# Kernel optimization log

Measured on AMD Instinct MI355X. Metric: run time of the kernel, lower is better.

## Reference

```python
import jax, jax.numpy as jnp
import numpy as np

EPS = 1e-4
LN_EPS = 1e-5
N, E, D_IN, D_HID, D_OUT = 100000, 1600000, 128, 256, 128


def _layer_norm(x, g, b):
    m = jnp.mean(x, axis=-1, keepdims=True)
    v = jnp.mean(jnp.square(x - m), axis=-1, keepdims=True)
    return (x - m) * jax.lax.rsqrt(v + LN_EPS) * g + b


def setup_inputs() -> dict:
    key = jax.random.key(0)
    ks = jax.random.split(key, 10)
    x = jax.random.normal(ks[0], (N, D_IN), dtype=jnp.float32)
    edge_index = jax.random.randint(ks[1], (2, E), 0, N, dtype=jnp.int64)
    degree = jax.random.uniform(ks[2], (N,), dtype=jnp.float32) * 32.0
    s_in = 1.0 / np.sqrt(D_IN)
    s_hid = 1.0 / np.sqrt(D_HID)
    return {
        "x": x,
        "edge_index": edge_index,
        "degree": degree,
        # fc: Linear(in_dim, out_dim, bias=True)
        "W_fc": jax.random.normal(ks[3], (D_OUT, D_IN), dtype=jnp.float32) * s_in,
        "b_fc": jnp.zeros((D_OUT,), dtype=jnp.float32),
        # rate: Linear(in_dim, out_dim, bias=False)
        "W_rate": jax.random.normal(ks[4], (D_OUT, D_IN), dtype=jnp.float32) * s_in,
        # rob_bound: Linear(in,hid)+Softplus -> Linear(hid,out) -> LayerNorm(out)
        "W1": jax.random.normal(ks[5], (D_HID, D_IN), dtype=jnp.float32) * s_in,
        "b1": jnp.zeros((D_HID,), dtype=jnp.float32),
        "W2": jax.random.normal(ks[6], (D_OUT, D_HID), dtype=jnp.float32) * s_hid,
        "b2": jnp.zeros((D_OUT,), dtype=jnp.float32),
        "ln1_g": jnp.ones((D_OUT,), dtype=jnp.float32),
        "ln1_b": jnp.zeros((D_OUT,), dtype=jnp.float32),
        # final self.norm LayerNorm(out)
        "ln2_g": jnp.ones((D_OUT,), dtype=jnp.float32),
        "ln2_b": jnp.zeros((D_OUT,), dtype=jnp.float32),
    }


def reference(x, edge_index, degree, W_fc, b_fc, W_rate, W1, b1, W2, b2,
              ln1_g, ln1_b, ln2_g, ln2_b):
    # rate = Softplus(x @ W_rate^T)   (dropout = identity in eval)
    rate = jax.nn.softplus(jnp.einsum('nd,od->no', x, W_rate))
    # gamma = LayerNorm(Softplus(x @ W1^T + b1) @ W2^T + b2)
    h = jax.nn.softplus(jnp.einsum('nd,hd->nh', x, W1) + b1)
    gamma = _layer_norm(jnp.einsum('nh,oh->no', h, W2) + b2, ln1_g, ln1_b)
    # z = fc(x)
    z = jnp.einsum('nd,od->no', x, W_fc) + b_fc
    row, col = edge_index[0], edge_index[1]
    # edge gather + scatter-sum back onto source nodes (row)
    msg = z[row] + z[col]                                   # [E, D_OUT]
    agg = jax.ops.segment_sum(msg, row, num_segments=N)     # [N, D_OUT]
    out = (rate * agg + gamma) / (1.0 + rate * degree[:, None] + EPS) - z
    out = _layer_norm(out, ln2_g, ln2_b)
    return out  # act = Identity, dropout = identity (eval)
```

## Files before the change

### kernel.cpp

```cpp
#include <hip/hip_runtime.h>
#include <hip/hip_bf16.h>
#include <stdint.h>


typedef __attribute__((ext_vector_type(8))) short  sh8;
typedef __attribute__((ext_vector_type(4))) float  f32x4;

__device__ __forceinline__ float softplus_fast(float v) {
    const float t = __expf(-fabsf(v));
    return fmaxf(v, 0.0f) + __logf(1.0f + t);
}
__device__ __forceinline__ unsigned short f2b(float f) {
    unsigned int u = __float_as_uint(f);
    u += 0x7fffu + ((u >> 16) & 1u);
    return (unsigned short)(u >> 16);
}
__device__ __forceinline__ float b2lo(unsigned int u) {
    return __uint_as_float(u << 16);
}
__device__ __forceinline__ float b2hi(unsigned int u) {
    return __uint_as_float(u & 0xffff0000u);
}

__global__ __launch_bounds__(256)
void convert_pad(const float* __restrict__ x, unsigned short* __restrict__ xb,
                 long long n_valid, long long n_total)
{
    long long i = ((long long)blockIdx.x * blockDim.x + threadIdx.x) * 8;
    const long long stride = (long long)gridDim.x * blockDim.x * 8;
    for (; i < n_total; i += stride) {
        sh8 o;
        if (i + 8 <= n_valid) {
            const float4 f0 = *(const float4*)(x + i);
            const float4 f1 = *(const float4*)(x + i + 4);
            o[0] = (short)f2b(f0.x); o[1] = (short)f2b(f0.y);
            o[2] = (short)f2b(f0.z); o[3] = (short)f2b(f0.w);
            o[4] = (short)f2b(f1.x); o[5] = (short)f2b(f1.y);
            o[6] = (short)f2b(f1.z); o[7] = (short)f2b(f1.w);
        } else {
            o = (sh8)(short)0;
        }
        *(sh8*)(xb + i) = o;
    }
}

__global__ __launch_bounds__(256)
void convert_weights(const float* __restrict__ Wfc, const float* __restrict__ Wrt,
                     const float* __restrict__ W1,  const float* __restrict__ W2,
                     unsigned short* __restrict__ wb)
{
    const int i = blockIdx.x * blockDim.x + threadIdx.x;
    float v;
    if (i < 16384)       v = Wfc[i];
    else if (i < 32768)  v = Wrt[i - 16384];
    else if (i < 65536)  v = W1[i - 32768];
    else                 v = W2[i - 65536];
    wb[i] = f2b(v);
}


__global__ __launch_bounds__(256)
void gemm_fused3(const unsigned short* __restrict__ A, const unsigned short* __restrict__ Wcat,
                 const float* __restrict__ b_fc, const float* __restrict__ b1,
                 unsigned short* __restrict__ zbuf, unsigned short* __restrict__ rbuf,
                 unsigned short* __restrict__ hbuf)
{
    __shared__ unsigned short As[128 * 64];
    __shared__ unsigned short Bs[128 * 64];
    const int tid  = threadIdx.x;
    const int lane = tid & 63;
    const int w    = tid >> 6;
    const int wr   = w >> 1, wc = w & 1;
    const int row0 = blockIdx.x * 128;
    const int by   = blockIdx.y;
    const int col0 = by * 128;
    const int K    = 128;

    f32x4 acc[4][4];
    const f32x4 vzero = {0.f, 0.f, 0.f, 0.f};
    #pragma unroll
    for (int m = 0; m < 4; ++m)
        #pragma unroll
        for (int n = 0; n < 4; ++n) acc[m][n] = vzero;

    for (int kt = 0; kt < K; kt += 64) {
        #pragma unroll
        for (int c = 0; c < 4; ++c) {
            const int idx = c * 256 + tid;
            const int row = idx >> 3;
            const int gs  = (idx & 7) ^ (row & 7);
            __builtin_amdgcn_global_load_lds(
                (const __attribute__((address_space(1))) void*)(A + (size_t)(row0 + row) * K + kt + gs * 8),
                (__attribute__((address_space(3))) void*)(As + idx * 8), 16, 0, 0);
        }
        #pragma unroll
        for (int c = 0; c < 4; ++c) {
            const int idx = c * 256 + tid;
            const int row = idx >> 3;
            const int gs  = (idx & 7) ^ (row & 7);
            __builtin_amdgcn_global_load_lds(
                (const __attribute__((address_space(1))) void*)(Wcat + (size_t)(col0 + row) * K + kt + gs * 8),
                (__attribute__((address_space(3))) void*)(Bs + idx * 8), 16, 0, 0);
        }
        __syncthreads();

        #pragma unroll
        for (int kk = 0; kk < 2; ++kk) {
            const int gg = kk * 4 + (lane >> 4);
            sh8 a[4], b[4];
            #pragma unroll
            for (int m = 0; m < 4; ++m) {
                const int r = wr * 64 + m * 16 + (lane & 15);
                a[m] = *(const sh8*)(As + r * 64 + ((gg ^ (r & 7)) << 3));
            }
            #pragma unroll
            for (int n = 0; n < 4; ++n) {
                const int r = wc * 64 + n * 16 + (lane & 15);
                b[n] = *(const sh8*)(Bs + r * 64 + ((gg ^ (r & 7)) << 3));
            }
            #pragma unroll
            for (int m = 0; m < 4; ++m)
                #pragma unroll
                for (int n = 0; n < 4; ++n)
                    acc[m][n] = __builtin_amdgcn_mfma_f32_16x16x32_bf16(a[m], b[n], acc[m][n], 0, 0, 0);
        }
        __syncthreads();
    }

    unsigned short* dst;
    int ldc, cbase, mode;
    if (by == 0)      { dst = zbuf; ldc = 128; cbase = 0;   mode = 0; }
    else if (by == 1) { dst = rbuf; ldc = 128; cbase = 0;   mode = 1; }
    else              { dst = hbuf; ldc = 256; cbase = col0 - 256; mode = 2; }

    float bs[4];
    #pragma unroll
    for (int n = 0; n < 4; ++n) {
        const int cw = col0 + wc * 64 + n * 16 + (lane & 15);
        bs[n] = (mode == 0) ? b_fc[cw] : (mode == 2 ? b1[cw - 256] : 0.0f);
    }
    #pragma unroll
    for (int m = 0; m < 4; ++m) {
        #pragma unroll
        for (int r = 0; r < 4; ++r) {
            const int grow = row0 + wr * 64 + m * 16 + (lane >> 4) * 4 + r;
            #pragma unroll
            for (int n = 0; n < 4; ++n) {
                const int cdst = cbase + wc * 64 + n * 16 + (lane & 15);
                float v = acc[m][n][r] + bs[n];
                if (mode != 0) v = softplus_fast(v);
                dst[(size_t)grow * ldc + cdst] = f2b(v);
            }
        }
    }
}

__global__ __launch_bounds__(256)
void gemm_gpre(const unsigned short* __restrict__ A, const unsigned short* __restrict__ W,
               const float* __restrict__ bias, unsigned short* __restrict__ C16)
{
    __shared__ unsigned short As[128 * 64];
    __shared__ unsigned short Bs[128 * 64];
    const int tid  = threadIdx.x;
    const int lane = tid & 63;
    const int w    = tid >> 6;
    const int wr   = w >> 1, wc = w & 1;
    const int row0 = blockIdx.x * 128;
    const int K    = 256;

    f32x4 acc[4][4];
    const f32x4 vzero = {0.f, 0.f, 0.f, 0.f};
    #pragma unroll
    for (int m = 0; m < 4; ++m)
        #pragma unroll
        for (int n = 0; n < 4; ++n) acc[m][n] = vzero;

    for (int kt = 0; kt < K; kt += 64) {
        #pragma unroll
        for (int c = 0; c < 4; ++c) {
            const int idx = c * 256 + tid;
            const int row = idx >> 3;
            const int gs  = (idx & 7) ^ (row & 7);
            __builtin_amdgcn_global_load_lds(
                (const __attribute__((address_space(1))) void*)(A + (size_t)(row0 + row) * K + kt + gs * 8),
                (__attribute__((address_space(3))) void*)(As + idx * 8), 16, 0, 0);
        }
        #pragma unroll
        for (int c = 0; c < 4; ++c) {
            const int idx = c * 256 + tid;
            const int row = idx >> 3;
            const int gs  = (idx & 7) ^ (row & 7);
            __builtin_amdgcn_global_load_lds(
                (const __attribute__((address_space(1))) void*)(W + (size_t)row * K + kt + gs * 8),
                (__attribute__((address_space(3))) void*)(Bs + idx * 8), 16, 0, 0);
        }
        __syncthreads();

        #pragma unroll
        for (int kk = 0; kk < 2; ++kk) {
            const int gg = kk * 4 + (lane >> 4);
            sh8 a[4], b[4];
            #pragma unroll
            for (int m = 0; m < 4; ++m) {
                const int r = wr * 64 + m * 16 + (lane & 15);
                a[m] = *(const sh8*)(As + r * 64 + ((gg ^ (r & 7)) << 3));
            }
            #pragma unroll
            for (int n = 0; n < 4; ++n) {
                const int r = wc * 64 + n * 16 + (lane & 15);
                b[n] = *(const sh8*)(Bs + r * 64 + ((gg ^ (r & 7)) << 3));
            }
            #pragma unroll
            for (int m = 0; m < 4; ++m)
                #pragma unroll
                for (int n = 0; n < 4; ++n)
                    acc[m][n] = __builtin_amdgcn_mfma_f32_16x16x32_bf16(a[m], b[n], acc[m][n], 0, 0, 0);
        }
        __syncthreads();
    }

    float bs[4];
    #pragma unroll
    for (int n = 0; n < 4; ++n)
        bs[n] = bias[wc * 64 + n * 16 + (lane & 15)];
    #pragma unroll
    for (int m = 0; m < 4; ++m) {
        #pragma unroll
        for (int r = 0; r < 4; ++r) {
            const int grow = row0 + wr * 64 + m * 16 + (lane >> 4) * 4 + r;
            #pragma unroll
            for (int n = 0; n < 4; ++n) {
                const int cdst = wc * 64 + n * 16 + (lane & 15);
                C16[(size_t)grow * 128 + cdst] = f2b(acc[m][n][r] + bs[n]);
            }
        }
    }
}

__global__ void count_edges(const int* __restrict__ ei, int E, int* __restrict__ cnt) {
    for (int e = blockIdx.x * blockDim.x + threadIdx.x; e < E; e += gridDim.x * blockDim.x)
        atomicAdd(&cnt[ei[e]], 1);
}

__global__ void scan_part(const int* __restrict__ cnt, int n, int* __restrict__ part) {
    __shared__ int sdata[256];
    const int base = blockIdx.x * 1024;
    int s = 0;
    for (int i = threadIdx.x; i < 1024; i += 256) {
        const int idx = base + i;
        s += (idx < n) ? cnt[idx] : 0;
    }
    sdata[threadIdx.x] = s;
    __syncthreads();
    for (int st = 128; st > 0; st >>= 1) {
        if (threadIdx.x < st) sdata[threadIdx.x] += sdata[threadIdx.x + st];
        __syncthreads();
    }
    if (threadIdx.x == 0) part[blockIdx.x] = sdata[0];
}

__global__ __launch_bounds__(256)
void scan_top(int* __restrict__ part, int nb) {
    __shared__ int sums[256];
    const int tid = threadIdx.x;
    int v[4]; int s = 0;
    #pragma unroll
    for (int i = 0; i < 4; ++i) {
        const int idx = tid * 4 + i;
        v[i] = (idx < nb) ? part[idx] : 0;
        s += v[i];
    }
    sums[tid] = s;
    __syncthreads();
    for (int st = 1; st < 256; st <<= 1) {
        const int t = (tid >= st) ? sums[tid - st] : 0;
        __syncthreads();
        sums[tid] += t;
        __syncthreads();
    }
    int excl = sums[tid] - s;
    #pragma unroll
    for (int i = 0; i < 4; ++i) {
        const int idx = tid * 4 + i;
        if (idx < nb) part[idx] = excl;
        excl += v[i];
    }
}

__global__ void scan_final(const int* __restrict__ cnt, int n,
                           const int* __restrict__ part, int* __restrict__ offs) {
    __shared__ int sums[256];
    const int tid = threadIdx.x;
    const int base = blockIdx.x * 1024 + tid * 4;
    int v[4]; int s = 0;
    #pragma unroll
    for (int i = 0; i < 4; ++i) {
        const int idx = base + i;
        v[i] = (idx < n) ? cnt[idx] : 0;
        s += v[i];
    }
    sums[tid] = s;
    __syncthreads();
    for (int st = 1; st < 256; st <<= 1) {
        const int t = (tid >= st) ? sums[tid - st] : 0;
        __syncthreads();
        sums[tid] += t;
        __syncthreads();
    }
    int excl = part[blockIdx.x] + sums[tid] - s;
    #pragma unroll
    for (int i = 0; i < 4; ++i) {
        const int idx = base + i;
        if (idx < n) offs[idx] = excl;
        excl += v[i];
    }
}

__global__ void fill_edges(const int* __restrict__ ei, int E, const int* __restrict__ offs,
                           int* __restrict__ cur, int* __restrict__ bucket) {
    for (int e = blockIdx.x * blockDim.x + threadIdx.x; e < E; e += gridDim.x * blockDim.x) {
        const int r = ei[e];
        const int p = atomicAdd(&cur[r], 1);
        bucket[offs[r] + p] = ei[E + e];
    }
}

__device__ __forceinline__ float wave_allreduce_sum(float v) {
    #pragma unroll
    for (int m = 1; m < 64; m <<= 1) v += __shfl_xor(v, m, 64);
    return v;
}

__global__ __launch_bounds__(256)
void final_fused(const unsigned short* __restrict__ zb, const unsigned short* __restrict__ rtb,
                 const unsigned short* __restrict__ gpb, const float* __restrict__ degree,
                 const int* __restrict__ cnt, const int* __restrict__ offs,
                 const int* __restrict__ bucket,
                 const float* __restrict__ ln1g, const float* __restrict__ ln1b,
                 const float* __restrict__ ln2g, const float* __restrict__ ln2b,
                 float* __restrict__ out, int n)
{
    const int lane = threadIdx.x & 63;
    const int node = blockIdx.x * 4 + (threadIdx.x >> 6);
    if (node >= n) return;

    const unsigned int uz = ((const unsigned int*)(zb  + (size_t)node * 128))[lane];
    const unsigned int ur = ((const unsigned int*)(rtb + (size_t)node * 128))[lane];
    const unsigned int ug = ((const unsigned int*)(gpb + (size_t)node * 128))[lane];
    const float zx = b2lo(uz), zy = b2hi(uz);
    const float rx = b2lo(ur), ry = b2hi(ur);
    const float px = b2lo(ug), py = b2hi(ug);

    float mean = wave_allreduce_sum(px + py) * (1.0f / 128.0f);
    float d0 = px - mean, d1 = py - mean;
    float var = wave_allreduce_sum(d0 * d0 + d1 * d1) * (1.0f / 128.0f);
    float rstd = rsqrtf(var + 1e-5f);
    const float2 g1 = ((const float2*)ln1g)[lane];
    const float2 b1 = ((const float2*)ln1b)[lane];
    const float gmx = d0 * rstd * g1.x + b1.x;
    const float gmy = d1 * rstd * g1.y + b1.y;

    const int c    = cnt[node];
    const int o0   = offs[node];
    const int jend = o0 + c;
    float ax = (float)c * zx, ay = (float)c * zy;
    float bx = 0.0f, by = 0.0f;
    int j = o0;
    for (; j + 4 <= jend; j += 4) {
        const int c0 = bucket[j + 0];
        const int c1 = bucket[j + 1];
        const int c2 = bucket[j + 2];
        const int c3 = bucket[j + 3];
        const unsigned int u0 = ((const unsigned int*)(zb + (size_t)c0 * 128))[lane];
        const unsigned int u1 = ((const unsigned int*)(zb + (size_t)c1 * 128))[lane];
        const unsigned int u2 = ((const unsigned int*)(zb + (size_t)c2 * 128))[lane];
        const unsigned int u3 = ((const unsigned int*)(zb + (size_t)c3 * 128))[lane];
        ax += b2lo(u0) + b2lo(u2);
        ay += b2hi(u0) + b2hi(u2);
        bx += b2lo(u1) + b2lo(u3);
        by += b2hi(u1) + b2hi(u3);
    }
    for (; j < jend; ++j) {
        const int c0 = bucket[j];
        const unsigned int u0 = ((const unsigned int*)(zb + (size_t)c0 * 128))[lane];
        ax += b2lo(u0);
        ay += b2hi(u0);
    }
    ax += bx; ay += by;

    const float dg = degree[node];
    float ox = (rx * ax + gmx) / (1.0f + rx * dg + 1e-4f) - zx;
    float oy = (ry * ay + gmy) / (1.0f + ry * dg + 1e-4f) - zy;

    mean = wave_allreduce_sum(ox + oy) * (1.0f / 128.0f);
    d0 = ox - mean; d1 = oy - mean;
    var = wave_allreduce_sum(d0 * d0 + d1 * d1) * (1.0f / 128.0f);
    rstd = rsqrtf(var + 1e-5f);
    const float2 g2 = ((const float2*)ln2g)[lane];
    const float2 b2 = ((const float2*)ln2b)[lane];
    float2 res;
    res.x = d0 * rstd * g2.x + b2.x;
    res.y = d1 * rstd * g2.y + b2.y;
    ((float2*)(out + (size_t)node * 128))[lane] = res;
}

extern "C" void kernel_launch(void* const* d_in, const int* in_sizes, int n_in,
                              void* d_out, int out_size, void* d_ws, size_t ws_size,
                              hipStream_t stream)
{
    const float* x    = (const float*)d_in[0];
    const int*   ei   = (const int*)  d_in[1];
    const float* deg  = (const float*)d_in[2];
    const float* W_fc = (const float*)d_in[3];
    const float* b_fc = (const float*)d_in[4];
    const float* W_rt = (const float*)d_in[5];
    const float* W1   = (const float*)d_in[6];
    const float* b1   = (const float*)d_in[7];
    const float* W2   = (const float*)d_in[8];
    const float* b2   = (const float*)d_in[9];
    const float* ln1g = (const float*)d_in[10];
    const float* ln1b = (const float*)d_in[11];
    const float* ln2g = (const float*)d_in[12];
    const float* ln2b = (const float*)d_in[13];

    const int N  = in_sizes[0] / 128;
    const int E  = in_sizes[1] / 2;
    const int N2 = ((N + 127) / 128) * 128;
    const int gx = N2 / 128;
    float* out = (float*)d_out;

    char* p = (char*)d_ws;
    unsigned short* xb  = (unsigned short*)p;  p += (size_t)N2 * 128 * 2;
    unsigned short* hb  = (unsigned short*)p;  p += (size_t)N2 * 256 * 2;
    unsigned short* zb  = (unsigned short*)p;  p += (size_t)N2 * 128 * 2;
    unsigned short* rtb = (unsigned short*)p;  p += (size_t)N2 * 128 * 2;
    unsigned short* gpb = (unsigned short*)p;  p += (size_t)N2 * 128 * 2;
    unsigned short* wb  = (unsigned short*)p;  p += 98304 * 2;
    int* cnt    = (int*)p;                     p += (size_t)N * sizeof(int);
    int* cur    = (int*)p;                     p += (size_t)N * sizeof(int);
    int* offs   = (int*)p;                     p += (size_t)(N + 1) * sizeof(int);
    int* part   = (int*)p;                     p += 1024 * sizeof(int);
    int* bucket = (int*)p;

    const int nb = (N + 1023) / 1024;

    hipMemsetAsync(cnt, 0, (size_t)2 * N * sizeof(int), stream);
    count_edges<<<2048, 256, 0, stream>>>(ei, E, cnt);
    scan_part <<<nb, 256, 0, stream>>>(cnt, N, part);
    scan_top  <<<1, 256, 0, stream>>>(part, nb);
    scan_final<<<nb, 256, 0, stream>>>(cnt, N, part, offs);
    fill_edges<<<2048, 256, 0, stream>>>(ei, E, offs, cur, bucket);

    convert_pad    <<<2048, 256, 0, stream>>>(x, xb, (long long)N * 128, (long long)N2 * 128);
    convert_weights<<<384, 256, 0, stream>>>(W_fc, W_rt, W1, W2, wb);

    gemm_fused3<<<dim3(gx, 4), 256, 0, stream>>>(xb, wb, b_fc, b1, zb, rtb, hb);
    gemm_gpre  <<<dim3(gx, 1), 256, 0, stream>>>(hb, wb + 65536, b2, gpb);

    final_fused<<<(N + 3) / 4, 256, 0, stream>>>(zb, rtb, gpb, deg, cnt, offs, bucket,
                                                 ln1g, ln1b, ln2g, ln2b, out, N);
}
```

Baseline: 450.0 us.

## Fuse fp32-to-bf16 input conversion into GEMM and reuse X tile across outputs

Removes the separate convert_pad kernel and its bf16 copy of x. The first GEMM now loads fp32 x directly, converts it to bf16 into a swizzled LDS tile once, and loops over the four 128-column weight panels inside one block instead of using a 4-wide grid y. This cuts a full read and write of the converted x and reads x once per row block. The cost is fewer blocks (gx instead of 4*gx), more LDS per block, and serialized panel work per block, which lowers occupancy and parallelism.

```diff
diff --git a/kernel.cpp b/kernel.cpp
--- a/kernel.cpp
+++ b/kernel.cpp
@@ -20,28 +20,6 @@
 }
 __device__ __forceinline__ float b2hi(unsigned int u) {
     return __uint_as_float(u & 0xffff0000u);
-}
-
-__global__ __launch_bounds__(256)
-void convert_pad(const float* __restrict__ x, unsigned short* __restrict__ xb,
-                 long long n_valid, long long n_total)
-{
-    long long i = ((long long)blockIdx.x * blockDim.x + threadIdx.x) * 8;
-    const long long stride = (long long)gridDim.x * blockDim.x * 8;
-    for (; i < n_total; i += stride) {
-        sh8 o;
-        if (i + 8 <= n_valid) {
-            const float4 f0 = *(const float4*)(x + i);
-            const float4 f1 = *(const float4*)(x + i + 4);
-            o[0] = (short)f2b(f0.x); o[1] = (short)f2b(f0.y);
-            o[2] = (short)f2b(f0.z); o[3] = (short)f2b(f0.w);
-            o[4] = (short)f2b(f1.x); o[5] = (short)f2b(f1.y);
-            o[6] = (short)f2b(f1.z); o[7] = (short)f2b(f1.w);
-        } else {
-            o = (sh8)(short)0;
-        }
-        *(sh8*)(xb + i) = o;
-    }
 }
 
 __global__ __launch_bounds__(256)
@@ -58,98 +36,108 @@
     wb[i] = f2b(v);
 }
 
-
 __global__ __launch_bounds__(256)
-void gemm_fused3(const unsigned short* __restrict__ A, const unsigned short* __restrict__ Wcat,
+void gemm_fused4(const float* __restrict__ x, const unsigned short* __restrict__ Wcat,
                  const float* __restrict__ b_fc, const float* __restrict__ b1,
                  unsigned short* __restrict__ zbuf, unsigned short* __restrict__ rbuf,
-                 unsigned short* __restrict__ hbuf)
+                 unsigned short* __restrict__ hbuf, int nrows)
 {
-    __shared__ unsigned short As[128 * 64];
+    __shared__ unsigned short Xs[128 * 128];
     __shared__ unsigned short Bs[128 * 64];
     const int tid  = threadIdx.x;
     const int lane = tid & 63;
     const int w    = tid >> 6;
     const int wr   = w >> 1, wc = w & 1;
     const int row0 = blockIdx.x * 128;
-    const int by   = blockIdx.y;
-    const int col0 = by * 128;
-    const int K    = 128;
-
-    f32x4 acc[4][4];
-    const f32x4 vzero = {0.f, 0.f, 0.f, 0.f};
-    #pragma unroll
-    for (int m = 0; m < 4; ++m)
-        #pragma unroll
-        for (int n = 0; n < 4; ++n) acc[m][n] = vzero;
-
-    for (int kt = 0; kt < K; kt += 64) {
-        #pragma unroll
-        for (int c = 0; c < 4; ++c) {
-            const int idx = c * 256 + tid;
-            const int row = idx >> 3;
-            const int gs  = (idx & 7) ^ (row & 7);
-            __builtin_amdgcn_global_load_lds(
-                (const __attribute__((address_space(1))) void*)(A + (size_t)(row0 + row) * K + kt + gs * 8),
-                (__attribute__((address_space(3))) void*)(As + idx * 8), 16, 0, 0);
-        }
-        #pragma unroll
-        for (int c = 0; c < 4; ++c) {
-            const int idx = c * 256 + tid;
-            const int row = idx >> 3;
-            const int gs  = (idx & 7) ^ (row & 7);
-            __builtin_amdgcn_global_load_lds(
-                (const __attribute__((address_space(1))) void*)(Wcat + (size_t)(col0 + row) * K + kt + gs * 8),
-                (__attribute__((address_space(3))) void*)(Bs + idx * 8), 16, 0, 0);
-        }
-        __syncthreads();
-
-        #pragma unroll
-        for (int kk = 0; kk < 2; ++kk) {
-            const int gg = kk * 4 + (lane >> 4);
-            sh8 a[4], b[4];
-            #pragma unroll
-            for (int m = 0; m < 4; ++m) {
-                const int r = wr * 64 + m * 16 + (lane & 15);
-                a[m] = *(const sh8*)(As + r * 64 + ((gg ^ (r & 7)) << 3));
-            }
-            #pragma unroll
-            for (int n = 0; n < 4; ++n) {
-                const int r = wc * 64 + n * 16 + (lane & 15);
-                b[n] = *(const sh8*)(Bs + r * 64 + ((gg ^ (r & 7)) << 3));
-            }
-            #pragma unroll
-            for (int m = 0; m < 4; ++m)
+
+    #pragma unroll
+    for (int c = 0; c < 8; ++c) {
+        const int idx = c * 256 + tid;
+        const int row = idx >> 4;
+        const int g   = idx & 15;
+        const int ga  = row0 + row;
+        sh8 v;
+        if (ga < nrows) {
+            const float4 f0 = *(const float4*)(x + (size_t)ga * 128 + g * 8);
+            const float4 f1 = *(const float4*)(x + (size_t)ga * 128 + g * 8 + 4);
+            v[0] = (short)f2b(f0.x); v[1] = (short)f2b(f0.y);
+            v[2] = (short)f2b(f0.z); v[3] = (short)f2b(f0.w);
+            v[4] = (short)f2b(f1.x); v[5] = (short)f2b(f1.y);
+            v[6] = (short)f2b(f1.z); v[7] = (short)f2b(f1.w);
+        } else {
+            v = (sh8)(short)0;
+        }
+        *(sh8*)(Xs + (row * 16 + (g ^ (row & 7))) * 8) = v;
+    }
+
+    for (int p = 0; p < 4; ++p) {
+        f32x4 acc[4][4];
+        const f32x4 vzero = {0.f, 0.f, 0.f, 0.f};
+        #pragma unroll
+        for (int m = 0; m < 4; ++m)
+            #pragma unroll
+            for (int n = 0; n < 4; ++n) acc[m][n] = vzero;
+
+        for (int kt = 0; kt < 128; kt += 64) {
+            __syncthreads();
+            #pragma unroll
+            for (int c = 0; c < 4; ++c) {
+                const int idx  = c * 256 + tid;
+                const int brow = idx >> 3;
+                const int gs   = (idx & 7) ^ (brow & 7);
+                __builtin_amdgcn_global_load_lds(
+                    (const __attribute__((address_space(1))) void*)(Wcat + (size_t)(p * 128 + brow) * 128 + kt + gs * 8),
+                    (__attribute__((address_space(3))) void*)(Bs + idx * 8), 16, 0, 0);
+            }
+            __syncthreads();
+
+            const int gb = kt >> 3;
+            #pragma unroll
+            for (int kk = 0; kk < 2; ++kk) {
+                const int gg = kk * 4 + (lane >> 4);
+                sh8 a[4], b[4];
                 #pragma unroll
-                for (int n = 0; n < 4; ++n)
-                    acc[m][n] = __builtin_amdgcn_mfma_f32_16x16x32_bf16(a[m], b[n], acc[m][n], 0, 0, 0);
-        }
-        __syncthreads();
-    }
-
-    unsigned short* dst;
-    int ldc, cbase, mode;
-    if (by == 0)      { dst = zbuf; ldc = 128; cbase = 0;   mode = 0; }
-    else if (by == 1) { dst = rbuf; ldc = 128; cbase = 0;   mode = 1; }
-    else              { dst = hbuf; ldc = 256; cbase = col0 - 256; mode = 2; }
-
-    float bs[4];
-    #pragma unroll
-    for (int n = 0; n < 4; ++n) {
-        const int cw = col0 + wc * 64 + n * 16 + (lane & 15);
-        bs[n] = (mode == 0) ? b_fc[cw] : (mode == 2 ? b1[cw - 256] : 0.0f);
-    }
-    #pragma unroll
-    for (int m = 0; m < 4; ++m) {
-        #pragma unroll
-        for (int r = 0; r < 4; ++r) {
-            const int grow = row0 + wr * 64 + m * 16 + (lane >> 4) * 4 + r;
-            #pragma unroll
-            for (int n = 0; n < 4; ++n) {
-                const int cdst = cbase + wc * 64 + n * 16 + (lane & 15);
-                float v = acc[m][n][r] + bs[n];
-                if (mode != 0) v = softplus_fast(v);
-                dst[(size_t)grow * ldc + cdst] = f2b(v);
+                for (int m = 0; m < 4; ++m) {
+                    const int r = wr * 64 + m * 16 + (lane & 15);
+                    a[m] = *(const sh8*)(Xs + (r * 16 + ((gb + gg) ^ (r & 7))) * 8);
+                }
+                #pragma unroll
+                for (int n = 0; n < 4; ++n) {
+                    const int r = wc * 64 + n * 16 + (lane & 15);
+                    b[n] = *(const sh8*)(Bs + r * 64 + ((gg ^ (r & 7)) << 3));
+                }
+                #pragma unroll
+                for (int m = 0; m < 4; ++m)
+                    #pragma unroll
+                    for (int n = 0; n < 4; ++n)
+                        acc[m][n] = __builtin_amdgcn_mfma_f32_16x16x32_bf16(a[m], b[n], acc[m][n], 0, 0, 0);
+            }
+        }
+
+        unsigned short* dst;
+        int ldc, cbase, sp;
+        if (p == 0)      { dst = zbuf; ldc = 128; cbase = 0;             sp = 0; }
+        else if (p == 1) { dst = rbuf; ldc = 128; cbase = 0;             sp = 1; }
+        else             { dst = hbuf; ldc = 256; cbase = (p - 2) * 128; sp = 1; }
+
+        float bs[4];
+        #pragma unroll
+        for (int n = 0; n < 4; ++n) {
+            const int cw = wc * 64 + n * 16 + (lane & 15);
+            bs[n] = (p == 0) ? b_fc[cw] : ((p >= 2) ? b1[cbase + cw] : 0.0f);
+        }
+        #pragma unroll
+        for (int m = 0; m < 4; ++m) {
+            #pragma unroll
+            for (int r = 0; r < 4; ++r) {
+                const int grow = row0 + wr * 64 + m * 16 + (lane >> 4) * 4 + r;
+                #pragma unroll
+                for (int n = 0; n < 4; ++n) {
+                    const int cdst = cbase + wc * 64 + n * 16 + (lane & 15);
+                    float v = acc[m][n][r] + bs[n];
+                    if (sp) v = softplus_fast(v);
+                    dst[(size_t)grow * ldc + cdst] = f2b(v);
+                }
             }
         }
     }
@@ -430,7 +418,6 @@
     float* out = (float*)d_out;
 
     char* p = (char*)d_ws;
-    unsigned short* xb  = (unsigned short*)p;  p += (size_t)N2 * 128 * 2;
     unsigned short* hb  = (unsigned short*)p;  p += (size_t)N2 * 256 * 2;
     unsigned short* zb  = (unsigned short*)p;  p += (size_t)N2 * 128 * 2;
     unsigned short* rtb = (unsigned short*)p;  p += (size_t)N2 * 128 * 2;
@@ -451,11 +438,10 @@
     scan_final<<<nb, 256, 0, stream>>>(cnt, N, part, offs);
     fill_edges<<<2048, 256, 0, stream>>>(ei, E, offs, cur, bucket);
 
-    convert_pad    <<<2048, 256, 0, stream>>>(x, xb, (long long)N * 128, (long long)N2 * 128);
     convert_weights<<<384, 256, 0, stream>>>(W_fc, W_rt, W1, W2, wb);
 
-    gemm_fused3<<<dim3(gx, 4), 256, 0, stream>>>(xb, wb, b_fc, b1, zb, rtb, hb);
-    gemm_gpre  <<<dim3(gx, 1), 256, 0, stream>>>(hb, wb + 65536, b2, gpb);
+    gemm_fused4<<<gx, 256, 0, stream>>>(x, wb, b_fc, b1, zb, rtb, hb, N);
+    gemm_gpre  <<<gx, 256, 0, stream>>>(hb, wb + 65536, b2, gpb);
 
     final_fused<<<(N + 3) / 4, 256, 0, stream>>>(zb, rtb, gpb, deg, cnt, offs, bucket,
                                                  ln1g, ln1b, ln2g, ln2b, out, N);
```

Result: no change. 442.7 us (-1.6%).
